# Kernel tuning notes

Hardware: AMD Instinct MI355X
Metric: run time of the kernel (lower is better)

Reference implementation:

```python
import jax, jax.numpy as jnp
import numpy as np

EPS = 1e-5

def layernorm(x, scale, bias):
    mu = jnp.mean(x, axis=-1, keepdims=True)
    var = jnp.var(x, axis=-1, keepdims=True)
    return (x - mu) * jax.lax.rsqrt(var + EPS) * scale + bias

def setup_inputs() -> dict:
    key = jax.random.key(0)
    ks = jax.random.split(key, 12)
    B, N, c_s, c_z, H = 1, 1024, 768, 128, 12
    sc = 1.0 / np.sqrt(c_s)
    inp = {
        "s": jax.random.normal(ks[0], (B, N, c_s), jnp.float32),
        "z": jax.random.normal(ks[1], (B, N, N, c_z), jnp.float32),
        "mask": jnp.ones((B, N), jnp.float32),
        "norm_s_scale": jnp.ones((c_s,), jnp.float32),
        "norm_s_bias": jnp.zeros((c_s,), jnp.float32),
        "Wq": jax.random.normal(ks[2], (c_s, c_s), jnp.float32) * sc,
        "bq": jax.random.normal(ks[3], (c_s,), jnp.float32) * 0.02,
        "Wk": jax.random.normal(ks[4], (c_s, c_s), jnp.float32) * sc,
        "Wv": jax.random.normal(ks[5], (c_s, c_s), jnp.float32) * sc,
        "Wg": jax.random.normal(ks[6], (c_s, c_s), jnp.float32) * sc,
        "norm_z_scale": jnp.ones((c_z,), jnp.float32),
        "norm_z_bias": jnp.zeros((c_z,), jnp.float32),
        "Wz": jax.random.normal(ks[7], (c_z, H), jnp.float32) / np.sqrt(c_z),
        "Wo": jax.random.normal(ks[8], (c_s, c_s), jnp.float32) * sc,  # zero-init in orig; random for nontrivial test
    }
    return inp

def reference(s, z, mask, norm_s_scale, norm_s_bias, Wq, bq, Wk, Wv, Wg,
              norm_z_scale, norm_z_bias, Wz, Wo):
    B, N, c_s = s.shape
    H = Wz.shape[1]
    D = c_s // H
    INF = 1000000.0
    sn = layernorm(s, norm_s_scale, norm_s_bias)                 # (B,N,c_s)
    q = (sn @ Wq + bq).reshape(B, N, H, D)
    k = (sn @ Wk).reshape(B, N, H, D)
    v = (sn @ Wv).reshape(B, N, H, D)
    g = jax.nn.sigmoid(sn @ Wg)                                  # (B,N,c_s)
    zb = jnp.einsum('bijc,ch->bhij', layernorm(z, norm_z_scale, norm_z_bias), Wz)
    attn = jnp.einsum('bihd,bjhd->bhij', q, k) / np.sqrt(D) + zb
    attn = attn + (1.0 - mask[:, None, None, :]) * -INF
    attn = jax.nn.softmax(attn, axis=-1)
    o = jnp.einsum('bhij,bjhd->bihd', attn, v).reshape(B, N, c_s)
    return (g * o) @ Wo
```

## Files before the change

kernel.cpp:

```cpp
#include <hip/hip_runtime.h>
#include <hip/hip_bf16.h>
#include <hip/hip_fp16.h>

#define CS 768
#define NTOK 1024
#define CZ 128
#define NH 12
#define HD 64
#define JC 8
#define ZHS 2184

typedef __attribute__((ext_vector_type(8))) short bf16x8;
typedef __attribute__((ext_vector_type(4))) float f32x4;
typedef __attribute__((ext_vector_type(8))) unsigned short ushort8_t;
typedef __attribute__((ext_vector_type(4))) unsigned short ushort4_t;

__device__ inline unsigned short f2bf(float f) {
  __hip_bfloat16 h = __float2bfloat16(f);
  return *reinterpret_cast<unsigned short*>(&h);
}
__device__ inline float bf2f(unsigned short u) {
  union { unsigned int i; float f; } c; c.i = ((unsigned int)u) << 16;
  return c.f;
}
__device__ inline unsigned int cvtpk_bf16(float lo, float hi) {
  unsigned int r;
  asm("v_cvt_pk_bf16_f32 %0, %1, %2" : "=v"(r) : "v"(lo), "v"(hi));
  return r;
}
__device__ inline unsigned int cvtpk_f16(float lo, float hi) {
  unsigned int r;
  asm("v_cvt_pkrtz_f16_f32 %0, %1, %2" : "=v"(r) : "v"(lo), "v"(hi));
  return r;
}

__global__ __launch_bounds__(256) void prep_kernel(const float* __restrict__ s,
    const float* __restrict__ sc, const float* __restrict__ bi, unsigned short* __restrict__ sn,
    const float* __restrict__ W0, const float* __restrict__ W1, const float* __restrict__ W2,
    const float* __restrict__ W3, const float* __restrict__ W4, unsigned short* __restrict__ wt) {
  __shared__ float tile[64][65];
  int tid = threadIdx.x;
  if (blockIdx.x < NTOK) {
    int row = blockIdx.x;
    const float* x = s + (size_t)row * CS;
    float v0 = x[tid], v1 = x[tid + 256], v2 = x[tid + 512];
    float sum = v0 + v1 + v2;
    float sq  = v0*v0 + v1*v1 + v2*v2;
    for (int off = 1; off < 64; off <<= 1) {
      sum += __shfl_xor(sum, off);
      sq  += __shfl_xor(sq,  off);
    }
    __shared__ float ws1[4], ws2[4];
    if ((tid & 63) == 0) { ws1[tid >> 6] = sum; ws2[tid >> 6] = sq; }
    __syncthreads();
    float S = ws1[0] + ws1[1] + ws1[2] + ws1[3];
    float Q = ws2[0] + ws2[1] + ws2[2] + ws2[3];
    float mu  = S * (1.f / CS);
    float var = Q * (1.f / CS) - mu * mu;
    float rs  = rsqrtf(var + 1e-5f);
    unsigned short* y = sn + (size_t)row * CS;
    y[tid]       = f2bf((v0 - mu) * rs * sc[tid]       + bi[tid]);
    y[tid + 256] = f2bf((v1 - mu) * rs * sc[tid + 256] + bi[tid + 256]);
    y[tid + 512] = f2bf((v2 - mu) * rs * sc[tid + 512] + bi[tid + 512]);
  } else {
    int bz = blockIdx.x - NTOK;
    int w = bz / 144, rem = bz % 144;
    int kt = rem % 12, nt = rem / 12;
    const float* W = w == 0 ? W0 : w == 1 ? W1 : w == 2 ? W2 : w == 3 ? W3 : W4;
    unsigned short* Wt = wt + (size_t)w * CS * CS;
    int k0 = kt * 64, n0 = nt * 64;
    #pragma unroll
    for (int it = 0; it < 4; ++it) {
      int r = (tid >> 4) + it * 16;
      int c = (tid & 15) * 4;
      float4 vv = *(const float4*)(W + (size_t)(k0 + r) * CS + n0 + c);
      tile[r][c] = vv.x; tile[r][c+1] = vv.y; tile[r][c+2] = vv.z; tile[r][c+3] = vv.w;
    }
    __syncthreads();
    #pragma unroll
    for (int it = 0; it < 2; ++it) {
      int idx = tid + it * 256;
      int n = idx >> 3, k8 = (idx & 7) * 8;
      ushort8_t o;
      #pragma unroll
      for (int e = 0; e < 8; ++e) o[e] = f2bf(tile[k8 + e][n]);
      *(ushort8_t*)(Wt + (size_t)(n0 + n) * CS + k0 + k8) = o;
    }
  }
}

__global__ __launch_bounds__(256) void qkvg_gemm(const unsigned short* __restrict__ A,
    const unsigned short* __restrict__ Wt, const float* __restrict__ bq,
    unsigned short* __restrict__ qb, unsigned short* __restrict__ kb,
    unsigned short* __restrict__ vtb, unsigned short* __restrict__ gbuf) {
  __shared__ __align__(16) unsigned short As[64][40];
  __shared__ __align__(16) unsigned short Bs[64][40];
  int tid = threadIdx.x;
  int wid = tid >> 6, lane = tid & 63;
  int lrow = lane & 15, lk8 = (lane >> 4) * 8;
  int row0 = blockIdx.y * 64, col0 = blockIdx.x * 64;
  int ar = tid >> 2, ak = (tid & 3) * 8;
  f32x4 acc[4] = {};
  for (int k0 = 0; k0 < CS; k0 += 32) {
    *(ushort8_t*)&As[ar][ak] = *(const ushort8_t*)(A  + (size_t)(row0 + ar) * CS + k0 + ak);
    *(ushort8_t*)&Bs[ar][ak] = *(const ushort8_t*)(Wt + (size_t)(col0 + ar) * CS + k0 + ak);
    __syncthreads();
    bf16x8 af = *(bf16x8*)&As[wid * 16 + lrow][lk8];
    #pragma unroll
    for (int nb = 0; nb < 4; ++nb) {
      bf16x8 bfr = *(bf16x8*)&Bs[nb * 16 + lrow][lk8];
      acc[nb] = __builtin_amdgcn_mfma_f32_16x16x32_bf16(af, bfr, acc[nb], 0, 0, 0);
    }
    __syncthreads();
  }
  int sect = col0 / CS;
  int ncol0 = col0 - sect * CS;
  int grow0 = row0 + wid * 16 + (lane >> 4) * 4;
  if (sect == 2) {
    int jperm0 = ((grow0 >> 5) << 5) + 8 * (lane >> 4) + 4 * (wid & 1);
    #pragma unroll
    for (int nb = 0; nb < 4; ++nb) {
      int dg = ncol0 + nb * 16 + lrow;
      ushort4_t o;
      #pragma unroll
      for (int r = 0; r < 4; ++r) o[r] = f2bf(acc[nb][r]);
      *(ushort4_t*)(vtb + (size_t)dg * NTOK + jperm0) = o;
    }
  } else {
    unsigned short* dst = sect == 0 ? qb : sect == 1 ? kb : gbuf;
    #pragma unroll
    for (int nb = 0; nb < 4; ++nb) {
      int gcol = ncol0 + nb * 16 + lrow;
      float bv = (sect == 0) ? bq[gcol] : 0.f;
      #pragma unroll
      for (int r = 0; r < 4; ++r) {
        float val = acc[nb][r] + bv;
        if (sect == 3) val = 1.f / (1.f + __expf(-val));
        dst[(size_t)(grow0 + r) * CS + gcol] = f2bf(val);
      }
    }
  }
}

__global__ __launch_bounds__(256) void zbflash_kernel(const float* __restrict__ z,
    const float* __restrict__ gs, const float* __restrict__ gb,
    const float* __restrict__ Wz, const float* __restrict__ mask,
    const unsigned short* __restrict__ qb, const unsigned short* __restrict__ kb,
    const unsigned short* __restrict__ vtb,
    float* __restrict__ Opart, float* __restrict__ lsum) {
  __shared__ __half zs[NH * ZHS];
  const int i0 = blockIdx.x * 16;
  const int jc = blockIdx.y;
  const int j0 = jc * 128;
  const int tid = threadIdx.x;
  const int w = tid >> 6, lane = tid & 63;
  const int il = lane & 15, qg = lane >> 4;
  const float QKS = 0.125f * 1.44269504f;

  bf16x8 whi[4], wlo[4];
  float bh = 0.f;
  #pragma unroll
  for (int m = 0; m < 4; ++m) {
    union { unsigned short u[8]; bf16x8 v; } hi, lo;
    #pragma unroll
    for (int e = 0; e < 8; ++e) {
      int c = 32 * m + 8 * qg + e;
      float wv = (il < NH) ? Wz[c * NH + il] : 0.f;
      bh = fmaf(gb[c], wv, bh);
      float wp = gs[c] * wv;
      unsigned short h = f2bf(wp);
      hi.u[e] = h;
      lo.u[e] = f2bf(wp - bf2f(h));
    }
    whi[m] = hi.v; wlo[m] = lo.v;
  }
  bh += __shfl_xor(bh, 16);
  bh += __shfl_xor(bh, 32);

  for (int it = 0; it < 32; ++it) {
    int group = w * 32 + it;
    int i_local = group >> 3;
    int jseg = group & 7;
    const float* zrow = z + ((size_t)(i0 + i_local) * NTOK + j0 + jseg * 16 + il) * CZ;
    float zv[32];
    #pragma unroll
    for (int m = 0; m < 4; ++m) {
      float4 a = *(const float4*)(zrow + 32 * m + 8 * qg);
      float4 b = *(const float4*)(zrow + 32 * m + 8 * qg + 4);
      zv[m*8+0] = a.x; zv[m*8+1] = a.y; zv[m*8+2] = a.z; zv[m*8+3] = a.w;
      zv[m*8+4] = b.x; zv[m*8+5] = b.y; zv[m*8+6] = b.z; zv[m*8+7] = b.w;
    }
    float sum = 0.f, sq = 0.f;
    #pragma unroll
    for (int e = 0; e < 32; ++e) { sum += zv[e]; sq = fmaf(zv[e], zv[e], sq); }
    sum += __shfl_xor(sum, 16); sum += __shfl_xor(sum, 32);
    sq  += __shfl_xor(sq,  16); sq  += __shfl_xor(sq,  32);
    float mu  = sum * (1.f / CZ);
    float var = sq * (1.f / CZ) - mu * mu;
    float rs  = rsqrtf(var + 1e-5f);
    float nmr = -mu * rs;
    f32x4 acc = {};
    #pragma unroll
    for (int m = 0; m < 4; ++m) {
      union { unsigned int u[4]; bf16x8 v; } hi;
      #pragma unroll
      for (int e2 = 0; e2 < 4; ++e2) {
        float n0 = fmaf(zv[m*8+e2*2],     rs, nmr);
        float n1 = fmaf(zv[m*8+e2*2 + 1], rs, nmr);
        hi.u[e2] = cvtpk_bf16(n0, n1);
      }
      acc = __builtin_amdgcn_mfma_f32_16x16x32_bf16(hi.v, whi[m], acc, 0, 0, 0);
      acc = __builtin_amdgcn_mfma_f32_16x16x32_bf16(hi.v, wlo[m], acc, 0, 0, 0);
    }
    if (il < NH) {
      int jl = jseg * 16 + 4 * qg;
      float4 mk = *(const float4*)(mask + j0 + jl);
      float o0 = (acc[0] + bh + (1.f - mk.x) * -1000000.0f) * 1.44269504f - 16.f;
      float o1 = (acc[1] + bh + (1.f - mk.y) * -1000000.0f) * 1.44269504f - 16.f;
      float o2 = (acc[2] + bh + (1.f - mk.z) * -1000000.0f) * 1.44269504f - 16.f;
      float o3 = (acc[3] + bh + (1.f - mk.w) * -1000000.0f) * 1.44269504f - 16.f;
      unsigned int p01 = cvtpk_f16(o0, o1);
      unsigned int p23 = cvtpk_f16(o2, o3);
      *(uint2*)(zs + il * ZHS + i_local * 136 + jl) = make_uint2(p01, p23);
    }
  }
  __syncthreads();

  const int irow = i0 + il;
  for (int hh = 0; hh < 3; ++hh) {
    const int h = w * 3 + hh;
    bf16x8 qf0 = *(const bf16x8*)(qb + (size_t)irow * CS + h * HD + qg * 8);
    bf16x8 qf1 = *(const bf16x8*)(qb + (size_t)irow * CS + h * HD + 32 + qg * 8);
    const __half* zh = zs + h * ZHS + il * 136;
    f32x4 oacc[4] = {};
    float plocal = 0.f;
    #pragma unroll
    for (int jt = 0; jt < 2; ++jt) {
      int jb0 = j0 + jt * 64;
      f32x4 sacc[4] = {};
      #pragma unroll
      for (int jb = 0; jb < 4; ++jb) {
        const unsigned short* kbase = kb + (size_t)(jb0 + jb * 16 + il) * CS + h * HD;
        bf16x8 kf0 = *(const bf16x8*)(kbase + qg * 8);
        bf16x8 kf1 = *(const bf16x8*)(kbase + 32 + qg * 8);
        sacc[jb] = __builtin_amdgcn_mfma_f32_16x16x32_bf16(kf0, qf0, sacc[jb], 0, 0, 0);
        sacc[jb] = __builtin_amdgcn_mfma_f32_16x16x32_bf16(kf1, qf1, sacc[jb], 0, 0, 0);
      }
      unsigned int c0[4], c1[4];
      #pragma unroll
      for (int jb = 0; jb < 4; ++jb) {
        uint2 zr = *(const uint2*)(zh + jt * 64 + jb * 16 + qg * 4);
        const __half2* hz = (const __half2*)&zr;
        float z0 = __low2float(hz[0]), z1 = __high2float(hz[0]);
        float z2 = __low2float(hz[1]), z3 = __high2float(hz[1]);
        float p0 = exp2f(fmaf(sacc[jb][0], QKS, z0));
        float p1 = exp2f(fmaf(sacc[jb][1], QKS, z1));
        float p2 = exp2f(fmaf(sacc[jb][2], QKS, z2));
        float p3 = exp2f(fmaf(sacc[jb][3], QKS, z3));
        plocal += (p0 + p1) + (p2 + p3);
        c0[jb] = cvtpk_bf16(p0, p1);
        c1[jb] = cvtpk_bf16(p2, p3);
      }
      #pragma unroll
      for (int js = 0; js < 2; ++js) {
        union { unsigned int u[4]; bf16x8 v; } pb;
        pb.u[0] = c0[2*js];
        pb.u[1] = c1[2*js];
        pb.u[2] = c0[2*js + 1];
        pb.u[3] = c1[2*js + 1];
        #pragma unroll
        for (int db = 0; db < 4; ++db) {
          bf16x8 vf = *(const bf16x8*)(vtb + (size_t)(h * HD + db * 16 + il) * NTOK + jb0 + js * 32 + qg * 8);
          oacc[db] = __builtin_amdgcn_mfma_f32_16x16x32_bf16(vf, pb.v, oacc[db], 0, 0, 0);
        }
      }
    }
    plocal += __shfl_xor(plocal, 16);
    plocal += __shfl_xor(plocal, 32);
    float* obase = Opart + ((size_t)(jc * NH + h) << 16) + ((size_t)irow << 6);
    #pragma unroll
    for (int db = 0; db < 4; ++db)
      *(float4*)(obase + db * 16 + qg * 4) = *(float4*)&oacc[db];
    if (qg == 0)
      lsum[((jc * NH + h) << 10) + irow] = plocal;
  }
}

__global__ __launch_bounds__(256) void combine_kernel(const float* __restrict__ Opart,
    const float* __restrict__ lsum, const unsigned short* __restrict__ gbuf,
    unsigned short* __restrict__ gob) {
  int t = threadIdx.x;
  int r = blockIdx.x * 4 + (t >> 6);
  int h = r >> 10, i = r & (NTOK - 1), d = t & 63;
  float ltot = 0.f;
  #pragma unroll
  for (int c = 0; c < JC; ++c) ltot += lsum[((c * NH + h) << 10) + i];
  float o = 0.f;
  #pragma unroll
  for (int c = 0; c < JC; ++c)
    o += Opart[((size_t)(c * NH + h) << 16) + ((size_t)i << 6) + d];
  float inv = 1.f / ltot;
  size_t off = (size_t)i * CS + h * HD + d;
  gob[off] = f2bf(o * inv * bf2f(gbuf[off]));
}

__global__ __launch_bounds__(256) void out_gemm(const unsigned short* __restrict__ A,
    const unsigned short* __restrict__ Bt, float* __restrict__ C) {
  __shared__ __align__(16) unsigned short As[64][40];
  __shared__ __align__(16) unsigned short Bs[64][40];
  int tid = threadIdx.x;
  int wid = tid >> 6, lane = tid & 63;
  int lrow = lane & 15, lk8 = (lane >> 4) * 8;
  int row0 = blockIdx.y * 64, col0 = blockIdx.x * 64;
  int ar = tid >> 2, ak = (tid & 3) * 8;
  f32x4 acc[4] = {};
  for (int k0 = 0; k0 < CS; k0 += 32) {
    *(ushort8_t*)&As[ar][ak] = *(const ushort8_t*)(A  + (size_t)(row0 + ar) * CS + k0 + ak);
    *(ushort8_t*)&Bs[ar][ak] = *(const ushort8_t*)(Bt + (size_t)(col0 + ar) * CS + k0 + ak);
    __syncthreads();
    bf16x8 af = *(bf16x8*)&As[wid * 16 + lrow][lk8];
    #pragma unroll
    for (int nb = 0; nb < 4; ++nb) {
      bf16x8 bfr = *(bf16x8*)&Bs[nb * 16 + lrow][lk8];
      acc[nb] = __builtin_amdgcn_mfma_f32_16x16x32_bf16(af, bfr, acc[nb], 0, 0, 0);
    }
    __syncthreads();
  }
  #pragma unroll
  for (int nb = 0; nb < 4; ++nb) {
    int gcol = col0 + nb * 16 + lrow;
    #pragma unroll
    for (int r = 0; r < 4; ++r) {
      int grow = row0 + wid * 16 + (lane >> 4) * 4 + r;
      C[(size_t)grow * CS + gcol] = acc[nb][r];
    }
  }
}

extern "C" void kernel_launch(void* const* d_in, const int* in_sizes, int n_in,
                              void* d_out, int out_size, void* d_ws, size_t ws_size,
                              hipStream_t stream) {
  const float* s    = (const float*)d_in[0];
  const float* z    = (const float*)d_in[1];
  const float* mask = (const float*)d_in[2];
  const float* nss  = (const float*)d_in[3];
  const float* nsb  = (const float*)d_in[4];
  const float* Wq   = (const float*)d_in[5];
  const float* bq   = (const float*)d_in[6];
  const float* Wk   = (const float*)d_in[7];
  const float* Wv   = (const float*)d_in[8];
  const float* Wg   = (const float*)d_in[9];
  const float* nzs  = (const float*)d_in[10];
  const float* nzb  = (const float*)d_in[11];
  const float* Wz   = (const float*)d_in[12];
  const float* Wo   = (const float*)d_in[13];
  float* out = (float*)d_out;

  const size_t SN = (size_t)NTOK * CS;
  const size_t WSZ = (size_t)CS * CS;

  float* Opart = (float*)d_ws;
  float* lsum  = Opart + (size_t)JC * NH * NTOK * HD;
  unsigned short* sn  = (unsigned short*)(lsum + (size_t)JC * NH * NTOK);
  unsigned short* qb  = sn  + SN;
  unsigned short* kb  = qb  + SN;
  unsigned short* vtb = kb  + SN;
  unsigned short* gbuf= vtb + SN;
  unsigned short* gob = gbuf+ SN;
  unsigned short* wt  = gob + SN;

  prep_kernel<<<NTOK + 720, 256, 0, stream>>>(s, nss, nsb, sn, Wq, Wk, Wv, Wg, Wo, wt);
  qkvg_gemm<<<dim3(48, 16), 256, 0, stream>>>(sn, wt, bq, qb, kb, vtb, gbuf);
  zbflash_kernel<<<dim3(64, JC), 256, 0, stream>>>(z, nzs, nzb, Wz, mask,
                                                   qb, kb, vtb, Opart, lsum);
  combine_kernel<<<NH * NTOK / 4, 256, 0, stream>>>(Opart, lsum, gbuf, gob);
  out_gemm<<<dim3(12, 16), 256, 0, stream>>>(gob, wt + 4 * WSZ, out);
}
```

Before: 176.1 us.

## Warp-specialize z-bias kernel into producer/consumer warps with double-buffered LDS

Rework the fused z-bias/flash kernel so each 512-thread block handles two key chunks. Four producer warps compute the layernormed z projection into one LDS buffer while four consumer warps run the attention MFMAs on the previous chunk from the other buffer, synchronized per stage. The intent is to overlap the memory-bound z streaming with the attention compute inside one block. In exchange, the LDS footprint doubles to about 105 KB of dynamic shared memory, which likely allows only one block per CU. The pipeline is also only three stages deep, so the first and last stages run without overlap.

```diff
diff --git a/kernel.cpp b/kernel.cpp
--- a/kernel.cpp
+++ b/kernel.cpp
@@ -142,147 +142,165 @@
   }
 }
 
-__global__ __launch_bounds__(256) void zbflash_kernel(const float* __restrict__ z,
+__global__ __launch_bounds__(512) void zbflash_kernel(const float* __restrict__ z,
     const float* __restrict__ gs, const float* __restrict__ gb,
     const float* __restrict__ Wz, const float* __restrict__ mask,
     const unsigned short* __restrict__ qb, const unsigned short* __restrict__ kb,
     const unsigned short* __restrict__ vtb,
     float* __restrict__ Opart, float* __restrict__ lsum) {
-  __shared__ __half zs[NH * ZHS];
-  const int i0 = blockIdx.x * 16;
-  const int jc = blockIdx.y;
-  const int j0 = jc * 128;
+  extern __shared__ __half zs[];
+  const int i0 = (blockIdx.x >> 2) * 16;
+  const int jc0 = (blockIdx.x & 3) * 2;
   const int tid = threadIdx.x;
   const int w = tid >> 6, lane = tid & 63;
   const int il = lane & 15, qg = lane >> 4;
   const float QKS = 0.125f * 1.44269504f;
+  const bool producer = (w < 4);
 
   bf16x8 whi[4], wlo[4];
   float bh = 0.f;
-  #pragma unroll
-  for (int m = 0; m < 4; ++m) {
-    union { unsigned short u[8]; bf16x8 v; } hi, lo;
-    #pragma unroll
-    for (int e = 0; e < 8; ++e) {
-      int c = 32 * m + 8 * qg + e;
-      float wv = (il < NH) ? Wz[c * NH + il] : 0.f;
-      bh = fmaf(gb[c], wv, bh);
-      float wp = gs[c] * wv;
-      unsigned short h = f2bf(wp);
-      hi.u[e] = h;
-      lo.u[e] = f2bf(wp - bf2f(h));
-    }
-    whi[m] = hi.v; wlo[m] = lo.v;
-  }
-  bh += __shfl_xor(bh, 16);
-  bh += __shfl_xor(bh, 32);
-
-  for (int it = 0; it < 32; ++it) {
-    int group = w * 32 + it;
-    int i_local = group >> 3;
-    int jseg = group & 7;
-    const float* zrow = z + ((size_t)(i0 + i_local) * NTOK + j0 + jseg * 16 + il) * CZ;
-    float zv[32];
+  if (producer) {
     #pragma unroll
     for (int m = 0; m < 4; ++m) {
-      float4 a = *(const float4*)(zrow + 32 * m + 8 * qg);
-      float4 b = *(const float4*)(zrow + 32 * m + 8 * qg + 4);
-      zv[m*8+0] = a.x; zv[m*8+1] = a.y; zv[m*8+2] = a.z; zv[m*8+3] = a.w;
-      zv[m*8+4] = b.x; zv[m*8+5] = b.y; zv[m*8+6] = b.z; zv[m*8+7] = b.w;
-    }
-    float sum = 0.f, sq = 0.f;
-    #pragma unroll
-    for (int e = 0; e < 32; ++e) { sum += zv[e]; sq = fmaf(zv[e], zv[e], sq); }
-    sum += __shfl_xor(sum, 16); sum += __shfl_xor(sum, 32);
-    sq  += __shfl_xor(sq,  16); sq  += __shfl_xor(sq,  32);
-    float mu  = sum * (1.f / CZ);
-    float var = sq * (1.f / CZ) - mu * mu;
-    float rs  = rsqrtf(var + 1e-5f);
-    float nmr = -mu * rs;
-    f32x4 acc = {};
-    #pragma unroll
-    for (int m = 0; m < 4; ++m) {
-      union { unsigned int u[4]; bf16x8 v; } hi;
+      union { unsigned short u[8]; bf16x8 v; } hi, lo;
       #pragma unroll
-      for (int e2 = 0; e2 < 4; ++e2) {
-        float n0 = fmaf(zv[m*8+e2*2],     rs, nmr);
-        float n1 = fmaf(zv[m*8+e2*2 + 1], rs, nmr);
-        hi.u[e2] = cvtpk_bf16(n0, n1);
+      for (int e = 0; e < 8; ++e) {
+        int c = 32 * m + 8 * qg + e;
+        float wv = (il < NH) ? Wz[c * NH + il] : 0.f;
+        bh = fmaf(gb[c], wv, bh);
+        float wp = gs[c] * wv;
+        unsigned short h = f2bf(wp);
+        hi.u[e] = h;
+        lo.u[e] = f2bf(wp - bf2f(h));
       }
-      acc = __builtin_amdgcn_mfma_f32_16x16x32_bf16(hi.v, whi[m], acc, 0, 0, 0);
-      acc = __builtin_amdgcn_mfma_f32_16x16x32_bf16(hi.v, wlo[m], acc, 0, 0, 0);
-    }
-    if (il < NH) {
-      int jl = jseg * 16 + 4 * qg;
-      float4 mk = *(const float4*)(mask + j0 + jl);
-      float o0 = (acc[0] + bh + (1.f - mk.x) * -1000000.0f) * 1.44269504f - 16.f;
-      float o1 = (acc[1] + bh + (1.f - mk.y) * -1000000.0f) * 1.44269504f - 16.f;
-      float o2 = (acc[2] + bh + (1.f - mk.z) * -1000000.0f) * 1.44269504f - 16.f;
-      float o3 = (acc[3] + bh + (1.f - mk.w) * -1000000.0f) * 1.44269504f - 16.f;
-      unsigned int p01 = cvtpk_f16(o0, o1);
-      unsigned int p23 = cvtpk_f16(o2, o3);
-      *(uint2*)(zs + il * ZHS + i_local * 136 + jl) = make_uint2(p01, p23);
-    }
-  }
-  __syncthreads();
-
-  const int irow = i0 + il;
-  for (int hh = 0; hh < 3; ++hh) {
-    const int h = w * 3 + hh;
-    bf16x8 qf0 = *(const bf16x8*)(qb + (size_t)irow * CS + h * HD + qg * 8);
-    bf16x8 qf1 = *(const bf16x8*)(qb + (size_t)irow * CS + h * HD + 32 + qg * 8);
-    const __half* zh = zs + h * ZHS + il * 136;
-    f32x4 oacc[4] = {};
-    float plocal = 0.f;
-    #pragma unroll
-    for (int jt = 0; jt < 2; ++jt) {
-      int jb0 = j0 + jt * 64;
-      f32x4 sacc[4] = {};
-      #pragma unroll
-      for (int jb = 0; jb < 4; ++jb) {
-        const unsigned short* kbase = kb + (size_t)(jb0 + jb * 16 + il) * CS + h * HD;
-        bf16x8 kf0 = *(const bf16x8*)(kbase + qg * 8);
-        bf16x8 kf1 = *(const bf16x8*)(kbase + 32 + qg * 8);
-        sacc[jb] = __builtin_amdgcn_mfma_f32_16x16x32_bf16(kf0, qf0, sacc[jb], 0, 0, 0);
-        sacc[jb] = __builtin_amdgcn_mfma_f32_16x16x32_bf16(kf1, qf1, sacc[jb], 0, 0, 0);
-      }
-      unsigned int c0[4], c1[4];
-      #pragma unroll
-      for (int jb = 0; jb < 4; ++jb) {
-        uint2 zr = *(const uint2*)(zh + jt * 64 + jb * 16 + qg * 4);
-        const __half2* hz = (const __half2*)&zr;
-        float z0 = __low2float(hz[0]), z1 = __high2float(hz[0]);
-        float z2 = __low2float(hz[1]), z3 = __high2float(hz[1]);
-        float p0 = exp2f(fmaf(sacc[jb][0], QKS, z0));
-        float p1 = exp2f(fmaf(sacc[jb][1], QKS, z1));
-        float p2 = exp2f(fmaf(sacc[jb][2], QKS, z2));
-        float p3 = exp2f(fmaf(sacc[jb][3], QKS, z3));
-        plocal += (p0 + p1) + (p2 + p3);
-        c0[jb] = cvtpk_bf16(p0, p1);
-        c1[jb] = cvtpk_bf16(p2, p3);
-      }
-      #pragma unroll
-      for (int js = 0; js < 2; ++js) {
-        union { unsigned int u[4]; bf16x8 v; } pb;
-        pb.u[0] = c0[2*js];
-        pb.u[1] = c1[2*js];
-        pb.u[2] = c0[2*js + 1];
-        pb.u[3] = c1[2*js + 1];
-        #pragma unroll
-        for (int db = 0; db < 4; ++db) {
-          bf16x8 vf = *(const bf16x8*)(vtb + (size_t)(h * HD + db * 16 + il) * NTOK + jb0 + js * 32 + qg * 8);
-          oacc[db] = __builtin_amdgcn_mfma_f32_16x16x32_bf16(vf, pb.v, oacc[db], 0, 0, 0);
+      whi[m] = hi.v; wlo[m] = lo.v;
+    }
+    bh += __shfl_xor(bh, 16);
+    bh += __shfl_xor(bh, 32);
+  }
+
+  for (int k = 0; k < 3; ++k) {
+    if (producer) {
+      if (k < 2) {
+        const int jc = jc0 + k;
+        const int j0 = jc * 128;
+        __half* zbuf = zs + (size_t)(k & 1) * NH * ZHS;
+        const int pw = w;
+        for (int it = 0; it < 32; ++it) {
+          int group = pw * 32 + it;
+          int i_local = group >> 3;
+          int jseg = group & 7;
+          const float* zrow = z + ((size_t)(i0 + i_local) * NTOK + j0 + jseg * 16 + il) * CZ;
+          float zv[32];
+          #pragma unroll
+          for (int m = 0; m < 4; ++m) {
+            float4 a = *(const float4*)(zrow + 32 * m + 8 * qg);
+            float4 b = *(const float4*)(zrow + 32 * m + 8 * qg + 4);
+            zv[m*8+0] = a.x; zv[m*8+1] = a.y; zv[m*8+2] = a.z; zv[m*8+3] = a.w;
+            zv[m*8+4] = b.x; zv[m*8+5] = b.y; zv[m*8+6] = b.z; zv[m*8+7] = b.w;
+          }
+          float sum = 0.f, sq = 0.f;
+          #pragma unroll
+          for (int e = 0; e < 32; ++e) { sum += zv[e]; sq = fmaf(zv[e], zv[e], sq); }
+          sum += __shfl_xor(sum, 16); sum += __shfl_xor(sum, 32);
+          sq  += __shfl_xor(sq,  16); sq  += __shfl_xor(sq,  32);
+          float mu  = sum * (1.f / CZ);
+          float var = sq * (1.f / CZ) - mu * mu;
+          float rs  = rsqrtf(var + 1e-5f);
+          float nmr = -mu * rs;
+          f32x4 acc = {};
+          #pragma unroll
+          for (int m = 0; m < 4; ++m) {
+            union { unsigned int u[4]; bf16x8 v; } hi;
+            #pragma unroll
+            for (int e2 = 0; e2 < 4; ++e2) {
+              float n0 = fmaf(zv[m*8+e2*2],     rs, nmr);
+              float n1 = fmaf(zv[m*8+e2*2 + 1], rs, nmr);
+              hi.u[e2] = cvtpk_bf16(n0, n1);
+            }
+            acc = __builtin_amdgcn_mfma_f32_16x16x32_bf16(hi.v, whi[m], acc, 0, 0, 0);
+            acc = __builtin_amdgcn_mfma_f32_16x16x32_bf16(hi.v, wlo[m], acc, 0, 0, 0);
+          }
+          if (il < NH) {
+            int jl = jseg * 16 + 4 * qg;
+            float4 mk = *(const float4*)(mask + j0 + jl);
+            float o0 = (acc[0] + bh + (1.f - mk.x) * -1000000.0f) * 1.44269504f - 16.f;
+            float o1 = (acc[1] + bh + (1.f - mk.y) * -1000000.0f) * 1.44269504f - 16.f;
+            float o2 = (acc[2] + bh + (1.f - mk.z) * -1000000.0f) * 1.44269504f - 16.f;
+            float o3 = (acc[3] + bh + (1.f - mk.w) * -1000000.0f) * 1.44269504f - 16.f;
+            unsigned int p01 = cvtpk_f16(o0, o1);
+            unsigned int p23 = cvtpk_f16(o2, o3);
+            *(uint2*)(zbuf + il * ZHS + i_local * 136 + jl) = make_uint2(p01, p23);
+          }
         }
       }
-    }
-    plocal += __shfl_xor(plocal, 16);
-    plocal += __shfl_xor(plocal, 32);
-    float* obase = Opart + ((size_t)(jc * NH + h) << 16) + ((size_t)irow << 6);
-    #pragma unroll
-    for (int db = 0; db < 4; ++db)
-      *(float4*)(obase + db * 16 + qg * 4) = *(float4*)&oacc[db];
-    if (qg == 0)
-      lsum[((jc * NH + h) << 10) + irow] = plocal;
+    } else {
+      if (k >= 1) {
+        const int jc = jc0 + (k - 1);
+        const int j0 = jc * 128;
+        const __half* zsrc = zs + (size_t)((k - 1) & 1) * NH * ZHS;
+        const int cw = w - 4;
+        const int irow = i0 + il;
+        for (int hh = 0; hh < 3; ++hh) {
+          const int h = cw * 3 + hh;
+          bf16x8 qf0 = *(const bf16x8*)(qb + (size_t)irow * CS + h * HD + qg * 8);
+          bf16x8 qf1 = *(const bf16x8*)(qb + (size_t)irow * CS + h * HD + 32 + qg * 8);
+          const __half* zh = zsrc + h * ZHS + il * 136;
+          f32x4 oacc[4] = {};
+          float plocal = 0.f;
+          #pragma unroll
+          for (int jt = 0; jt < 2; ++jt) {
+            int jb0 = j0 + jt * 64;
+            f32x4 sacc[4] = {};
+            #pragma unroll
+            for (int jb = 0; jb < 4; ++jb) {
+              const unsigned short* kbase = kb + (size_t)(jb0 + jb * 16 + il) * CS + h * HD;
+              bf16x8 kf0 = *(const bf16x8*)(kbase + qg * 8);
+              bf16x8 kf1 = *(const bf16x8*)(kbase + 32 + qg * 8);
+              sacc[jb] = __builtin_amdgcn_mfma_f32_16x16x32_bf16(kf0, qf0, sacc[jb], 0, 0, 0);
+              sacc[jb] = __builtin_amdgcn_mfma_f32_16x16x32_bf16(kf1, qf1, sacc[jb], 0, 0, 0);
+            }
+            unsigned int c0[4], c1[4];
+            #pragma unroll
+            for (int jb = 0; jb < 4; ++jb) {
+              uint2 zr = *(const uint2*)(zh + jt * 64 + jb * 16 + qg * 4);
+              const __half2* hz = (const __half2*)&zr;
+              float z0 = __low2float(hz[0]), z1 = __high2float(hz[0]);
+              float z2 = __low2float(hz[1]), z3 = __high2float(hz[1]);
+              float p0 = exp2f(fmaf(sacc[jb][0], QKS, z0));
+              float p1 = exp2f(fmaf(sacc[jb][1], QKS, z1));
+              float p2 = exp2f(fmaf(sacc[jb][2], QKS, z2));
+              float p3 = exp2f(fmaf(sacc[jb][3], QKS, z3));
+              plocal += (p0 + p1) + (p2 + p3);
+              c0[jb] = cvtpk_bf16(p0, p1);
+              c1[jb] = cvtpk_bf16(p2, p3);
+            }
+            #pragma unroll
+            for (int js = 0; js < 2; ++js) {
+              union { unsigned int u[4]; bf16x8 v; } pb;
+              pb.u[0] = c0[2*js];
+              pb.u[1] = c1[2*js];
+              pb.u[2] = c0[2*js + 1];
+              pb.u[3] = c1[2*js + 1];
+              #pragma unroll
+              for (int db = 0; db < 4; ++db) {
+                bf16x8 vf = *(const bf16x8*)(vtb + (size_t)(h * HD + db * 16 + il) * NTOK + jb0 + js * 32 + qg * 8);
+                oacc[db] = __builtin_amdgcn_mfma_f32_16x16x32_bf16(vf, pb.v, oacc[db], 0, 0, 0);
+              }
+            }
+          }
+          plocal += __shfl_xor(plocal, 16);
+          plocal += __shfl_xor(plocal, 32);
+          float* obase = Opart + ((size_t)(jc * NH + h) << 16) + ((size_t)irow << 6);
+          #pragma unroll
+          for (int db = 0; db < 4; ++db)
+            *(float4*)(obase + db * 16 + qg * 4) = *(float4*)&oacc[db];
+          if (qg == 0)
+            lsum[((jc * NH + h) << 10) + irow] = plocal;
+        }
+      }
+    }
+    __syncthreads();
   }
 }
 
@@ -371,8 +389,8 @@
 
   prep_kernel<<<NTOK + 720, 256, 0, stream>>>(s, nss, nsb, sn, Wq, Wk, Wv, Wg, Wo, wt);
   qkvg_gemm<<<dim3(48, 16), 256, 0, stream>>>(sn, wt, bq, qb, kb, vtb, gbuf);
-  zbflash_kernel<<<dim3(64, JC), 256, 0, stream>>>(z, nzs, nzb, Wz, mask,
-                                                   qb, kb, vtb, Opart, lsum);
+  zbflash_kernel<<<256, 512, 2 * NH * ZHS * sizeof(__half), stream>>>(
+      z, nzs, nzb, Wz, mask, qb, kb, vtb, Opart, lsum);
   combine_kernel<<<NH * NTOK / 4, 256, 0, stream>>>(Opart, lsum, gbuf, gob);
   out_gemm<<<dim3(12, 16), 256, 0, stream>>>(gob, wt + 4 * WSZ, out);
 }
```

Result: slower. 189.6 us (+7.6%).
